# Performance work log

Measured on AMD Instinct MI355X. Metric: run time of the kernel, lower is better.

The kernel has to match this reference:

```python
import jax, jax.numpy as jnp
import numpy as np

MIN_BW = 0.1
MAX_BW = 10.0
BW_FACTOR = 1.0
SAMPLE = 512  # min(512, B) with B >= 512


def _pairwise_dist_sq(a, b):
    # ||a_i - b_j||^2 via GEMM: [N, M], avoids [N, M, D] intermediate
    a2 = jnp.sum(a * a, axis=-1)[:, None]
    b2 = jnp.sum(b * b, axis=-1)[None, :]
    d = a2 + b2 - 2.0 * (a @ b.T)
    return jnp.maximum(d, 0.0)


def _bandwidth(x, y):
    # torch: median heuristic on first SAMPLE rows, under no_grad
    xs = jax.lax.stop_gradient(x[:SAMPLE])
    ys = jax.lax.stop_gradient(y[:SAMPLE])
    dist_sq = _pairwise_dist_sq(xs, ys)
    bw_sq = jnp.median(dist_sq.reshape(-1))
    bw = jnp.sqrt(bw_sq / 2.0) * BW_FACTOR
    return jnp.clip(bw, MIN_BW, MAX_BW)


def setup_inputs() -> dict:
    key = jax.random.key(0)
    kx, ksx, ky, ksy = jax.random.split(key, 4)
    B, D = 4096, 512
    return {
        "x": jax.random.normal(kx, (B, D), dtype=jnp.float32),
        "score_x": jax.random.normal(ksx, (B, D), dtype=jnp.float32),
        "y": jax.random.normal(ky, (B, D), dtype=jnp.float32),
        "score_y": jax.random.normal(ksy, (B, D), dtype=jnp.float32),
    }


def reference(x, score_x, y, score_y):
    D = x.shape[-1]
    h = _bandwidth(x, y)
    h2 = h * h

    dist_sq = _pairwise_dist_sq(x, y)                      # [B, B]
    k = jnp.exp(-dist_sq / (2.0 * h2))                     # [B, B]

    # term1[i,j] = k[i,j] * <score_x_i, score_y_j>
    term1 = k * (score_x @ score_y.T)

    # term2[i,j] = <x_i - y_j, score_y_j> * k[i,j] / h^2
    term2 = ((x @ score_y.T) - jnp.sum(y * score_y, axis=-1)[None, :]) * k / h2

    # term3[i,j] = ||x_i - y_j||^2 * k / h^4 - k * D / h^2
    term3 = dist_sq * k / (h2 * h2) - k * (D / h2)

    return term1 + term2 + term3
```

## Files before the change

### kernel.cpp

```cpp
#include <hip/hip_runtime.h>
#include <hip/hip_bf16.h>

typedef __attribute__((ext_vector_type(8))) short bf16x8;
typedef __attribute__((ext_vector_type(4))) float f32x4;

#define B_N 4096
#define DIM 512
#define HBINS 8192

#define OFF_PARAMS 0
#define OFF_X2     256
#define OFF_Y2     16640
#define OFF_YSY    33024
#define OFF_HIST   49408
#define OFF_TILES  98304
#define MAT_ELEMS  2097152
#define WS_NEED    (OFF_TILES + (size_t)4 * MAT_ELEMS * 2)

static __device__ __forceinline__ unsigned short f2bf_rne(float f) {
    unsigned int u = __float_as_uint(f);
    u += 0x7FFFu + ((u >> 16) & 1u);
    return (unsigned short)(u >> 16);
}
static __device__ __forceinline__ float bf2f(unsigned short h) {
    return __uint_as_float(((unsigned int)h) << 16);
}

static __device__ __forceinline__ int swz(int r, int k) {
    return r * 32 + ((((k >> 3) ^ ((r >> 1) & 3))) << 3) + (k & 7);
}

__global__ __launch_bounds__(256) void k_hist2(
    const float* __restrict__ X, const float* __restrict__ Y,
    unsigned int* __restrict__ hist) {
    __shared__ __align__(16) unsigned short sA[2048];
    __shared__ __align__(16) unsigned short sB[2048];
    __shared__ unsigned int hloc[HBINS];
    __shared__ float x2s[64], y2s[64];

    int t = threadIdx.x;
    int bi = blockIdx.y, bj = blockIdx.x;
    for (int i = t; i < HBINS; i += 256) hloc[i] = 0;

    int lane = t & 63, w = t >> 6;
    int wm = w >> 1, wn = w & 1;
    int fr = lane & 15, fko = (lane >> 4) * 8;

    f32x4 axy[2][2];
#pragma unroll
    for (int i = 0; i < 2; ++i)
#pragma unroll
        for (int j = 0; j < 2; ++j) axy[i][j] = (f32x4)0.f;

    int r = t >> 2, k0 = (t & 3) * 8;
    const float* gx = X + (size_t)(bi * 64 + r) * DIM + k0;
    const float* gy = Y + (size_t)(bj * 64 + r) * DIM + k0;

    int ixA[2], ixB[2];
#pragma unroll
    for (int fm = 0; fm < 2; ++fm) ixA[fm] = swz(wm * 32 + fm * 16 + fr, fko);
#pragma unroll
    for (int fn = 0; fn < 2; ++fn) ixB[fn] = swz(wn * 32 + fn * 16 + fr, fko);

    float na = 0.f, nb = 0.f;
    float4 A0, A1, B0, B1;
#define LDK(kt_) do {                                                       \
        A0 = *(const float4*)(gx + (kt_) * 32);                             \
        A1 = *(const float4*)(gx + (kt_) * 32 + 4);                         \
        B0 = *(const float4*)(gy + (kt_) * 32);                             \
        B1 = *(const float4*)(gy + (kt_) * 32 + 4);                         \
    } while (0)

    LDK(0);
    for (int kt = 0; kt < 16; ++kt) {
        float av[8] = {A0.x, A0.y, A0.z, A0.w, A1.x, A1.y, A1.z, A1.w};
        float bv[8] = {B0.x, B0.y, B0.z, B0.w, B1.x, B1.y, B1.z, B1.w};
        bf16x8 ha, hb;
#pragma unroll
        for (int j = 0; j < 8; ++j) {
            na += av[j] * av[j];
            nb += bv[j] * bv[j];
            ha[j] = (short)f2bf_rne(av[j]);
            hb[j] = (short)f2bf_rne(bv[j]);
        }
        __syncthreads();
        *(bf16x8*)&sA[swz(r, k0)] = ha;
        *(bf16x8*)&sB[swz(r, k0)] = hb;
        if (kt < 15) LDK(kt + 1);
        __syncthreads();

        bf16x8 aX[2];
#pragma unroll
        for (int fm = 0; fm < 2; ++fm) aX[fm] = *(const bf16x8*)&sA[ixA[fm]];
#pragma unroll
        for (int fn = 0; fn < 2; ++fn) {
            bf16x8 bY = *(const bf16x8*)&sB[ixB[fn]];
#pragma unroll
            for (int fm = 0; fm < 2; ++fm)
                axy[fm][fn] = __builtin_amdgcn_mfma_f32_16x16x32_bf16(aX[fm], bY, axy[fm][fn], 0, 0, 0);
        }
    }
#undef LDK

    na += __shfl_xor(na, 1); na += __shfl_xor(na, 2);
    nb += __shfl_xor(nb, 1); nb += __shfl_xor(nb, 2);
    if ((t & 3) == 0) { x2s[r] = na; y2s[r] = nb; }
    __syncthreads();

    int fq = lane >> 4;
#pragma unroll
    for (int fm = 0; fm < 2; ++fm)
#pragma unroll
        for (int fn = 0; fn < 2; ++fn)
#pragma unroll
            for (int rr = 0; rr < 4; ++rr) {
                int rl = wm * 32 + fm * 16 + fq * 4 + rr;
                int cl = wn * 32 + fn * 16 + fr;
                float d = fmaxf(x2s[rl] + y2s[cl] - 2.0f * axy[fm][fn][rr], 0.0f);
                int bin = (int)(d * 4.0f);
                if (bin > HBINS - 1) bin = HBINS - 1;
                atomicAdd(&hloc[bin], 1u);
            }
    __syncthreads();
    for (int i = t; i < HBINS; i += 256) {
        unsigned int v = hloc[i];
        if (v) atomicAdd(&hist[i], v);
    }
}

__global__ __launch_bounds__(256, 1) void k_median(
    const unsigned int* __restrict__ hist, float* __restrict__ params) {
    __shared__ unsigned int hsum[HBINS];
    __shared__ unsigned int part[256];
    __shared__ float vv[2];
    int t = threadIdx.x;
    for (int i = t; i < HBINS / 4; i += 256)
        ((uint4*)hsum)[i] = ((const uint4*)hist)[i];
    __syncthreads();
    unsigned int s = 0;
#pragma unroll 8
    for (int b = t * 32; b < t * 32 + 32; ++b) s += hsum[b];
    part[t] = s;
    __syncthreads();
    unsigned int pre = 0;
    for (int i = 0; i < 256; ++i) {
        unsigned int v = part[i];
        if (i < t) pre += v;
    }
    const unsigned int kk1 = 131072u, kk2 = 131073u;
    unsigned int hi = pre + s;
#pragma unroll
    for (int sel = 0; sel < 2; ++sel) {
        unsigned int kk = sel ? kk2 : kk1;
        if (kk > pre && kk <= hi) {
            unsigned int cc = pre;
            for (int b = 0; b < 32; ++b) {
                cc += hsum[t * 32 + b];
                if (cc >= kk) { vv[sel] = ((float)(t * 32 + b) + 0.5f) * 0.25f; break; }
            }
        }
    }
    __syncthreads();
    if (t == 0) {
        float med = 0.5f * (vv[0] + vv[1]);
        float bw = sqrtf(med * 0.5f);
        bw = fminf(fmaxf(bw, 0.1f), 10.0f);
        float h2 = bw * bw;
        params[0] = 1.0f / (2.0f * h2);
        params[1] = 1.0f / h2;
        params[2] = 1.0f / (h2 * h2);
        params[3] = (float)DIM / h2;
    }
}

__global__ void k_prestats(const float* __restrict__ X, const float* __restrict__ SX,
                           const float* __restrict__ Y, const float* __restrict__ SY,
                           const float* __restrict__ params, unsigned short* __restrict__ tiles,
                           float* __restrict__ x2, float* __restrict__ y2,
                           float* __restrict__ ysy) {
    int side = blockIdx.z;
    const float* P = side ? Y : X;
    const float* Q = side ? SY : SX;
    float c1 = side ? 0.0f : params[1];
    int tile = blockIdx.x, t = threadIdx.x;
    int r = t >> 1;
    int kt = blockIdx.y * 2 + (t & 1);
    const float* gp = P + (size_t)(tile * 128 + r) * DIM + kt * 32;
    const float* gq = Q + (size_t)(tile * 128 + r) * DIM + kt * 32;
    unsigned short* d0 = tiles + (size_t)side * 2 * MAT_ELEMS + (size_t)(tile * 16 + kt) * 4096;
    unsigned short* d1 = d0 + MAT_ELEMS;
    int rt = r >> 4, frl = r & 15;
    float s1 = 0.f, s2 = 0.f;
#pragma unroll
    for (int g = 0; g < 4; ++g) {
        float4 p0 = *(const float4*)(gp + g * 8);
        float4 p1 = *(const float4*)(gp + g * 8 + 4);
        float4 q0 = *(const float4*)(gq + g * 8);
        float4 q1 = *(const float4*)(gq + g * 8 + 4);
        float pv[8] = {p0.x, p0.y, p0.z, p0.w, p1.x, p1.y, p1.z, p1.w};
        float qv[8] = {q0.x, q0.y, q0.z, q0.w, q1.x, q1.y, q1.z, q1.w};
        bf16x8 h0, h1;
#pragma unroll
        for (int j = 0; j < 8; ++j) {
            s1 += pv[j] * pv[j];
            s2 += pv[j] * qv[j];
            h0[j] = (short)f2bf_rne(pv[j]);
            h1[j] = (short)f2bf_rne(qv[j] + c1 * pv[j]);
        }
        *(bf16x8*)&d0[swz(r, g * 8)] = h0;
        *(bf16x8*)&d1[rt * 512 + (g * 16 + frl) * 8] = h1;
    }
    s1 += __shfl_xor(s1, 1);
    s2 += __shfl_xor(s2, 1);
    if ((t & 1) == 0) {
        if (side == 0) {
            atomicAdd(&x2[tile * 128 + r], s1);
        } else {
            atomicAdd(&y2[tile * 128 + r], s1);
            atomicAdd(&ysy[tile * 128 + r], s2);
        }
    }
}

#define GLD(g, l) __builtin_amdgcn_global_load_lds(                                   \
    (const __attribute__((address_space(1))) void*)(g),                               \
    (__attribute__((address_space(3))) void*)(l), 16, 0, 0)

__global__ __launch_bounds__(256, 2) void k_main(
    const unsigned short* __restrict__ tiles,
    const float* __restrict__ x2g, const float* __restrict__ y2g,
    const float* __restrict__ ysyg, const float* __restrict__ params,
    float* __restrict__ out) {
    __shared__ __align__(16) unsigned short sA[2][4096];
    __shared__ __align__(16) unsigned short sB[2][4096];
    __shared__ float x2s[128], y2s[128], ysys[128];

    int t = threadIdx.x;
    int bm = blockIdx.y, bn = blockIdx.x;
    if (t < 128) x2s[t] = x2g[bm * 128 + t];
    else { y2s[t - 128] = y2g[bn * 128 + (t - 128)]; ysys[t - 128] = ysyg[bn * 128 + (t - 128)]; }
    __syncthreads();

    int lane = t & 63, w = t >> 6;
    int wm = w >> 1, wn = w & 1;
    int fr = lane & 15, fko = (lane >> 4) * 8;

    f32x4 axy[4][4], acb[4][4];
#pragma unroll
    for (int i = 0; i < 4; ++i)
#pragma unroll
        for (int j = 0; j < 4; ++j) { axy[i][j] = (f32x4)0.f; acb[i][j] = (f32x4)0.f; }

    const unsigned short* gaX = tiles + (size_t)(bm * 16) * 4096 + t * 8;
    const unsigned short* gbY = tiles + (size_t)2 * MAT_ELEMS + (size_t)(bn * 16) * 4096 + t * 8;
    const unsigned short* gaC = tiles + (size_t)MAT_ELEMS + (size_t)(bm * 16) * 4096
                              + (wm * 4) * 512 + lane * 8;
    const unsigned short* gbS = tiles + (size_t)3 * MAT_ELEMS + (size_t)(bn * 16) * 4096
                              + (wn * 4) * 512 + lane * 8;

#define STAGE(buf, kt_) do {                                                     \
        const unsigned short* pa_ = gaX + (size_t)(kt_) * 4096;                  \
        const unsigned short* pb_ = gbY + (size_t)(kt_) * 4096;                  \
        GLD(pa_,        &sA[buf][t * 8]);                                        \
        GLD(pa_ + 2048, &sA[buf][2048 + t * 8]);                                 \
        GLD(pb_,        &sB[buf][t * 8]);                                        \
        GLD(pb_ + 2048, &sB[buf][2048 + t * 8]);                                 \
    } while (0)

#define FRAGLD(dC, dS, kt_) do {                                                 \
        const unsigned short* pc_ = gaC + (size_t)(kt_) * 4096;                  \
        const unsigned short* ps_ = gbS + (size_t)(kt_) * 4096;                  \
        dC[0] = *(const bf16x8*)(pc_);        dS[0] = *(const bf16x8*)(ps_);     \
        dC[1] = *(const bf16x8*)(pc_ + 512);  dS[1] = *(const bf16x8*)(ps_ + 512);\
        dC[2] = *(const bf16x8*)(pc_ + 1024); dS[2] = *(const bf16x8*)(ps_ + 1024);\
        dC[3] = *(const bf16x8*)(pc_ + 1536); dS[3] = *(const bf16x8*)(ps_ + 1536);\
    } while (0)

    int ixA[4], ixB[4];
#pragma unroll
    for (int fm = 0; fm < 4; ++fm) ixA[fm] = swz(wm * 64 + fm * 16 + fr, fko);
#pragma unroll
    for (int fn = 0; fn < 4; ++fn) ixB[fn] = swz(wn * 64 + fn * 16 + fr, fko);

    bf16x8 fC0[4], fS0[4], fC1[4], fS1[4];

#define KSTEP(CB, CURC, CURS, NXTC, NXTS, NKT, DOPF) do {                        \
        asm volatile("s_waitcnt vmcnt(8)" ::: "memory");   \
        __builtin_amdgcn_sched_barrier(0);                                       \
        __builtin_amdgcn_s_barrier();                                            \
        bf16x8 dX[4], dY[4];                                                     \
        dX[0] = *(const bf16x8*)&sA[CB][ixA[0]];                                 \
        dX[1] = *(const bf16x8*)&sA[CB][ixA[1]];                                 \
        dX[2] = *(const bf16x8*)&sA[CB][ixA[2]];                                 \
        dX[3] = *(const bf16x8*)&sA[CB][ixA[3]];                                 \
        dY[0] = *(const bf16x8*)&sB[CB][ixB[0]];                                 \
        dY[1] = *(const bf16x8*)&sB[CB][ixB[1]];                                 \
        dY[2] = *(const bf16x8*)&sB[CB][ixB[2]];                                 \
        dY[3] = *(const bf16x8*)&sB[CB][ixB[3]];                                 \
        asm volatile("s_waitcnt lgkmcnt(0)" ::: "memory");                       \
        __builtin_amdgcn_sched_barrier(0);                                       \
        __builtin_amdgcn_s_barrier();         \
        if (DOPF) {                                                              \
            STAGE(CB ^ 1, NKT);                                                  \
            FRAGLD(NXTC, NXTS, NKT);                                             \
            asm volatile("s_waitcnt vmcnt(12)" ::: "memory"); \
        } else {                                                                 \
            asm volatile("s_waitcnt vmcnt(0)" ::: "memory");                     \
        }                                                                        \
        __builtin_amdgcn_sched_barrier(0);                                       \
        _Pragma("unroll")                                                        \
        for (int fn_ = 0; fn_ < 4; ++fn_) {                                      \
            _Pragma("unroll")                                                    \
            for (int fm_ = 0; fm_ < 4; ++fm_) {                                  \
                axy[fm_][fn_] = __builtin_amdgcn_mfma_f32_16x16x32_bf16(         \
                    dX[fm_], dY[fn_], axy[fm_][fn_], 0, 0, 0);                   \
                acb[fm_][fn_] = __builtin_amdgcn_mfma_f32_16x16x32_bf16(         \
                    CURC[fm_], CURS[fn_], acb[fm_][fn_], 0, 0, 0);               \
            }                                                                    \
        }                                                                        \
    } while (0)

    STAGE(0, 0);
    FRAGLD(fC0, fS0, 0);

    for (int k2 = 0; k2 < 7; ++k2) {
        KSTEP(0, fC0, fS0, fC1, fS1, 2 * k2 + 1, 1);
        KSTEP(1, fC1, fS1, fC0, fS0, 2 * k2 + 2, 1);
    }
    KSTEP(0, fC0, fS0, fC1, fS1, 15, 1);
    KSTEP(1, fC1, fS1, fC0, fS0, 0, 0);
#undef KSTEP
#undef STAGE
#undef FRAGLD

    float c0 = params[0], c1 = params[1], c2 = params[2], c3 = params[3];
    int fq = lane >> 4;
#pragma unroll
    for (int fm = 0; fm < 4; ++fm) {
#pragma unroll
        for (int fn = 0; fn < 4; ++fn) {
#pragma unroll
            for (int r = 0; r < 4; ++r) {
                int rl = wm * 64 + fm * 16 + fq * 4 + r;
                int cl = wn * 64 + fn * 16 + fr;
                float d = fmaxf(x2s[rl] + y2s[cl] - 2.0f * axy[fm][fn][r], 0.0f);
                float kv = __expf(-d * c0);
                out[(size_t)(bm * 128 + rl) * B_N + (bn * 128 + cl)] =
                    kv * (acb[fm][fn][r] - c1 * ysys[cl] + d * c2 - c3);
            }
        }
    }
}

__global__ void k_rowstats(const float* __restrict__ X, const float* __restrict__ Y,
                           const float* __restrict__ SY,
                           float* __restrict__ x2, float* __restrict__ y2,
                           float* __restrict__ ysy) {
    int t = threadIdx.x;
    int r = blockIdx.x * 4 + (t >> 6);
    int lane = t & 63;
    const float4* px = (const float4*)(X + (size_t)r * DIM) + lane * 2;
    const float4* py = (const float4*)(Y + (size_t)r * DIM) + lane * 2;
    const float4* ps = (const float4*)(SY + (size_t)r * DIM) + lane * 2;
    float4 a0 = px[0], a1 = px[1];
    float4 b0 = py[0], b1 = py[1];
    float4 c0 = ps[0], c1 = ps[1];
    float s1 = a0.x*a0.x + a0.y*a0.y + a0.z*a0.z + a0.w*a0.w
             + a1.x*a1.x + a1.y*a1.y + a1.z*a1.z + a1.w*a1.w;
    float s2 = b0.x*b0.x + b0.y*b0.y + b0.z*b0.z + b0.w*b0.w
             + b1.x*b1.x + b1.y*b1.y + b1.z*b1.z + b1.w*b1.w;
    float s3 = b0.x*c0.x + b0.y*c0.y + b0.z*c0.z + b0.w*c0.w
             + b1.x*c1.x + b1.y*c1.y + b1.z*c1.z + b1.w*c1.w;
#pragma unroll
    for (int o = 32; o > 0; o >>= 1) {
        s1 += __shfl_down(s1, o);
        s2 += __shfl_down(s2, o);
        s3 += __shfl_down(s3, o);
    }
    if (lane == 0) { x2[r] = s1; y2[r] = s2; ysy[r] = s3; }
}

__global__ void k_hist_fp32(const float* __restrict__ X, const float* __restrict__ Y,
                            const float* __restrict__ x2, const float* __restrict__ y2,
                            unsigned int* __restrict__ hist) {
    __shared__ float xs[32][68];
    __shared__ float ys[32][68];
    __shared__ unsigned int hloc[HBINS];
    int t = threadIdx.x;
    for (int i = t; i < HBINS; i += 256) hloc[i] = 0;
    int i0 = blockIdx.y * 32, j0 = blockIdx.x * 32;
    float a00 = 0.f, a01 = 0.f, a10 = 0.f, a11 = 0.f;
    int ti = (t >> 4) * 2, tj = (t & 15) * 2;
    for (int c = 0; c < 8; ++c) {
        __syncthreads();
        int rr = t >> 3, cc = (t & 7) * 8;
        const float* gx = X + (size_t)(i0 + rr) * DIM + c * 64 + cc;
        *(float4*)&xs[rr][cc] = *(const float4*)gx;
        *(float4*)&xs[rr][cc + 4] = *(const float4*)(gx + 4);
        const float* gy = Y + (size_t)(j0 + rr) * DIM + c * 64 + cc;
        *(float4*)&ys[rr][cc] = *(const float4*)gy;
        *(float4*)&ys[rr][cc + 4] = *(const float4*)(gy + 4);
        __syncthreads();
        for (int kk = 0; kk < 64; ++kk) {
            float a0 = xs[ti][kk], a1 = xs[ti + 1][kk];
            float b0 = ys[tj][kk], b1 = ys[tj + 1][kk];
            a00 += a0 * b0; a01 += a0 * b1; a10 += a1 * b0; a11 += a1 * b1;
        }
    }
    float s[2][2] = {{a00, a01}, {a10, a11}};
#pragma unroll
    for (int ii = 0; ii < 2; ++ii)
#pragma unroll
        for (int jj = 0; jj < 2; ++jj) {
            float d = fmaxf(x2[i0 + ti + ii] + y2[j0 + tj + jj] - 2.f * s[ii][jj], 0.f);
            int bin = (int)(d * 4.0f);
            if (bin > HBINS - 1) bin = HBINS - 1;
            atomicAdd(&hloc[bin], 1u);
        }
    __syncthreads();
    for (int i = t; i < HBINS; i += 256) {
        unsigned int v = hloc[i];
        if (v) atomicAdd(&hist[i], v);
    }
}

static __device__ __forceinline__ void store_hi(unsigned short* tile, int r, int k0,
                                                float4 v0, float4 v1) {
    bf16x8 h;
    h[0] = (short)f2bf_rne(v0.x); h[1] = (short)f2bf_rne(v0.y);
    h[2] = (short)f2bf_rne(v0.z); h[3] = (short)f2bf_rne(v0.w);
    h[4] = (short)f2bf_rne(v1.x); h[5] = (short)f2bf_rne(v1.y);
    h[6] = (short)f2bf_rne(v1.z); h[7] = (short)f2bf_rne(v1.w);
    *(bf16x8*)&tile[swz(r, k0)] = h;
}
static __device__ __forceinline__ void store_hilo(unsigned short* th, unsigned short* tl,
                                                  int r, int k0, float4 v0, float4 v1) {
    float f[8] = {v0.x, v0.y, v0.z, v0.w, v1.x, v1.y, v1.z, v1.w};
    bf16x8 h, l;
#pragma unroll
    for (int j = 0; j < 8; ++j) {
        unsigned short hh = f2bf_rne(f[j]);
        h[j] = (short)hh;
        l[j] = (short)f2bf_rne(f[j] - bf2f(hh));
    }
    *(bf16x8*)&th[swz(r, k0)] = h;
    *(bf16x8*)&tl[swz(r, k0)] = l;
}

__global__ __launch_bounds__(256, 2) void k_main_fb(
    const float* __restrict__ X, const float* __restrict__ SX,
    const float* __restrict__ Y, const float* __restrict__ SY,
    const float* __restrict__ x2g, const float* __restrict__ y2g,
    const float* __restrict__ ysyg, const float* __restrict__ params,
    float* __restrict__ out) {
    __shared__ __align__(16) unsigned short tX[4096];
    __shared__ __align__(16) unsigned short tSXH[4096];
    __shared__ __align__(16) unsigned short tSXL[4096];
    __shared__ __align__(16) unsigned short tY[2048];
    __shared__ __align__(16) unsigned short tSYH[2048];
    __shared__ __align__(16) unsigned short tSYL[2048];
    __shared__ float x2s[128];
    __shared__ float y2s[64];
    __shared__ float ysys[64];

    int t = threadIdx.x;
    int bm = blockIdx.y, bn = blockIdx.x;
    if (t < 128) x2s[t] = x2g[bm * 128 + t];
    else if (t < 192) y2s[t - 128] = y2g[bn * 64 + (t - 128)];
    else ysys[t - 192] = ysyg[bn * 64 + (t - 192)];

    int lane = t & 63, w = t >> 6, wm = w >> 1, wn = w & 1;
    f32x4 axy[4][2], ass[4][2], axsy[4][2];
#pragma unroll
    for (int i = 0; i < 4; ++i)
#pragma unroll
        for (int j = 0; j < 2; ++j) {
            axy[i][j] = (f32x4)0.f; ass[i][j] = (f32x4)0.f; axsy[i][j] = (f32x4)0.f;
        }

    for (int kt = 0; kt < DIM / 32; ++kt) {
        int kb = kt * 32;
#pragma unroll
        for (int h = 0; h < 2; ++h) {
            int s = t + h * 256;
            int r = s >> 2, k0 = (s & 3) * 8;
            const float* gx = X + (size_t)(bm * 128 + r) * DIM + kb + k0;
            store_hi(tX, r, k0, *(const float4*)gx, *(const float4*)(gx + 4));
            const float* gs = SX + (size_t)(bm * 128 + r) * DIM + kb + k0;
            store_hilo(tSXH, tSXL, r, k0, *(const float4*)gs, *(const float4*)(gs + 4));
        }
        {
            int r = t >> 2, k0 = (t & 3) * 8;
            const float* gy = Y + (size_t)(bn * 64 + r) * DIM + kb + k0;
            store_hi(tY, r, k0, *(const float4*)gy, *(const float4*)(gy + 4));
            const float* gq = SY + (size_t)(bn * 64 + r) * DIM + kb + k0;
            store_hilo(tSYH, tSYL, r, k0, *(const float4*)gq, *(const float4*)(gq + 4));
        }
        __syncthreads();

        int fr = lane & 15, fk = (lane >> 4) * 8;
        bf16x8 aX[4], aSH[4], aSL[4];
#pragma unroll
        for (int fm = 0; fm < 4; ++fm) {
            int ix = swz(wm * 64 + fm * 16 + fr, fk);
            aX[fm] = *(const bf16x8*)&tX[ix];
            aSH[fm] = *(const bf16x8*)&tSXH[ix];
            aSL[fm] = *(const bf16x8*)&tSXL[ix];
        }
#pragma unroll
        for (int fn = 0; fn < 2; ++fn) {
            int iy = swz(wn * 32 + fn * 16 + fr, fk);
            bf16x8 bY = *(const bf16x8*)&tY[iy];
            bf16x8 bH = *(const bf16x8*)&tSYH[iy];
            bf16x8 bL = *(const bf16x8*)&tSYL[iy];
#pragma unroll
            for (int fm = 0; fm < 4; ++fm) {
                axy[fm][fn] = __builtin_amdgcn_mfma_f32_16x16x32_bf16(aX[fm], bY, axy[fm][fn], 0, 0, 0);
                ass[fm][fn] = __builtin_amdgcn_mfma_f32_16x16x32_bf16(aSH[fm], bH, ass[fm][fn], 0, 0, 0);
                ass[fm][fn] = __builtin_amdgcn_mfma_f32_16x16x32_bf16(aSH[fm], bL, ass[fm][fn], 0, 0, 0);
                ass[fm][fn] = __builtin_amdgcn_mfma_f32_16x16x32_bf16(aSL[fm], bH, ass[fm][fn], 0, 0, 0);
                axsy[fm][fn] = __builtin_amdgcn_mfma_f32_16x16x32_bf16(aX[fm], bH, axsy[fm][fn], 0, 0, 0);
            }
        }
        __syncthreads();
    }

    float c0 = params[0], c1 = params[1], c2 = params[2], c3 = params[3];
    int fr = lane & 15, fq = lane >> 4;
#pragma unroll
    for (int fm = 0; fm < 4; ++fm)
#pragma unroll
        for (int fn = 0; fn < 2; ++fn)
#pragma unroll
            for (int r = 0; r < 4; ++r) {
                int rl = wm * 64 + fm * 16 + fq * 4 + r;
                int cl = wn * 32 + fn * 16 + fr;
                float d = fmaxf(x2s[rl] + y2s[cl] - 2.0f * axy[fm][fn][r], 0.0f);
                float kv = __expf(-d * c0);
                out[(size_t)(bm * 128 + rl) * B_N + (bn * 64 + cl)] =
                    kv * ass[fm][fn][r] + (axsy[fm][fn][r] - ysys[cl]) * (kv * c1)
                    + d * kv * c2 - kv * c3;
            }
}

extern "C" void kernel_launch(void* const* d_in, const int* in_sizes, int n_in,
                              void* d_out, int out_size, void* d_ws, size_t ws_size,
                              hipStream_t stream) {
    const float* x  = (const float*)d_in[0];
    const float* sx = (const float*)d_in[1];
    const float* y  = (const float*)d_in[2];
    const float* sy = (const float*)d_in[3];
    float* out = (float*)d_out;
    char* ws = (char*)d_ws;
    float* params = (float*)(ws + OFF_PARAMS);
    float* x2 = (float*)(ws + OFF_X2);
    float* y2 = (float*)(ws + OFF_Y2);
    float* ysy = (float*)(ws + OFF_YSY);
    unsigned int* hist = (unsigned int*)(ws + OFF_HIST);
    unsigned short* tiles = (unsigned short*)(ws + OFF_TILES);

    if (ws_size >= WS_NEED) {
        hipMemsetAsync(ws + OFF_X2, 0, 3 * 16384 + HBINS * 4, stream);
        k_hist2<<<dim3(8, 8), dim3(256), 0, stream>>>(x, y, hist);
        k_median<<<1, 256, 0, stream>>>(hist, params);
        k_prestats<<<dim3(32, 8, 2), dim3(256), 0, stream>>>(x, sx, y, sy, params, tiles,
                                                             x2, y2, ysy);
        k_main<<<dim3(32, 32), dim3(256), 0, stream>>>(tiles, x2, y2, ysy, params, out);
    } else {
        hipMemsetAsync(hist, 0, HBINS * 4, stream);
        k_rowstats<<<B_N / 4, 256, 0, stream>>>(x, y, sy, x2, y2, ysy);
        k_hist_fp32<<<dim3(16, 16), dim3(256), 0, stream>>>(x, y, x2, y2, hist);
        k_median<<<1, 256, 0, stream>>>(hist, params);
        k_main_fb<<<dim3(64, 32), dim3(256), 0, stream>>>(x, sx, y, sy, x2, y2, ysy, params, out);
    }
}
```

Measured before the change: 93.54 us.

## Coalesce prestats tile writes and issue next-stage prefetch before LDS reads

The prestats kernel is restructured so each thread writes contiguous 16-byte chunks of the destination tiles, with the source index permuted to match the swizzle. Loads of the score operand are skipped where they are not needed, and row sums are reduced across four lanes. In the main GEMM loop, the next stage's global-to-LDS copy and fragment loads are issued right after the first barrier, before the current LDS reads, removing the second barrier. The MFMA block is wrapped in raised wave priority. The early prefetch relies on the double buffer staying race-free with only one barrier per step.

```diff
diff --git a/kernel.cpp b/kernel.cpp
--- a/kernel.cpp
+++ b/kernel.cpp
@@ -183,41 +183,80 @@
     const float* Q = side ? SY : SX;
     float c1 = side ? 0.0f : params[1];
     int tile = blockIdx.x, t = threadIdx.x;
-    int r = t >> 1;
-    int kt = blockIdx.y * 2 + (t & 1);
-    const float* gp = P + (size_t)(tile * 128 + r) * DIM + kt * 32;
-    const float* gq = Q + (size_t)(tile * 128 + r) * DIM + kt * 32;
-    unsigned short* d0 = tiles + (size_t)side * 2 * MAT_ELEMS + (size_t)(tile * 16 + kt) * 4096;
-    unsigned short* d1 = d0 + MAT_ELEMS;
-    int rt = r >> 4, frl = r & 15;
-    float s1 = 0.f, s2 = 0.f;
-#pragma unroll
-    for (int g = 0; g < 4; ++g) {
-        float4 p0 = *(const float4*)(gp + g * 8);
-        float4 p1 = *(const float4*)(gp + g * 8 + 4);
-        float4 q0 = *(const float4*)(gq + g * 8);
-        float4 q1 = *(const float4*)(gq + g * 8 + 4);
-        float pv[8] = {p0.x, p0.y, p0.z, p0.w, p1.x, p1.y, p1.z, p1.w};
-        float qv[8] = {q0.x, q0.y, q0.z, q0.w, q1.x, q1.y, q1.z, q1.w};
-        bf16x8 h0, h1;
-#pragma unroll
-        for (int j = 0; j < 8; ++j) {
-            s1 += pv[j] * pv[j];
-            s2 += pv[j] * qv[j];
-            h0[j] = (short)f2bf_rne(pv[j]);
-            h1[j] = (short)f2bf_rne(qv[j] + c1 * pv[j]);
-        }
-        *(bf16x8*)&d0[swz(r, g * 8)] = h0;
-        *(bf16x8*)&d1[rt * 512 + (g * 16 + frl) * 8] = h1;
-    }
-    s1 += __shfl_xor(s1, 1);
-    s2 += __shfl_xor(s2, 1);
-    if ((t & 1) == 0) {
-        if (side == 0) {
-            atomicAdd(&x2[tile * 128 + r], s1);
-        } else {
-            atomicAdd(&y2[tile * 128 + r], s1);
-            atomicAdd(&ysy[tile * 128 + r], s2);
+    unsigned short* base0 = tiles + (size_t)side * 2 * MAT_ELEMS;
+    unsigned short* base1 = base0 + MAT_ELEMS;
+
+#pragma unroll
+    for (int kt2 = 0; kt2 < 2; ++kt2) {
+        int kt = blockIdx.y * 2 + kt2;
+        unsigned short* d0 = base0 + (size_t)(tile * 16 + kt) * 4096;
+        unsigned short* d1 = base1 + (size_t)(tile * 16 + kt) * 4096;
+
+#pragma unroll
+        for (int c = 0; c < 2; ++c) {
+            int u = c * 256 + t;
+            int r = u >> 2;
+            int k = (((u & 3) ^ ((u >> 3) & 3))) << 3;
+            const float* gp = P + (size_t)(tile * 128 + r) * DIM + kt * 32 + k;
+            float4 p0 = *(const float4*)gp;
+            float4 p1 = *(const float4*)(gp + 4);
+            float pv[8] = {p0.x, p0.y, p0.z, p0.w, p1.x, p1.y, p1.z, p1.w};
+            float s1 = 0.f, s2 = 0.f;
+            bf16x8 h0;
+            if (side) {
+                const float* gq = Q + (size_t)(tile * 128 + r) * DIM + kt * 32 + k;
+                float4 q0 = *(const float4*)gq;
+                float4 q1 = *(const float4*)(gq + 4);
+                float qv[8] = {q0.x, q0.y, q0.z, q0.w, q1.x, q1.y, q1.z, q1.w};
+#pragma unroll
+                for (int j = 0; j < 8; ++j) {
+                    s1 += pv[j] * pv[j];
+                    s2 += pv[j] * qv[j];
+                    h0[j] = (short)f2bf_rne(pv[j]);
+                }
+            } else {
+#pragma unroll
+                for (int j = 0; j < 8; ++j) {
+                    s1 += pv[j] * pv[j];
+                    h0[j] = (short)f2bf_rne(pv[j]);
+                }
+            }
+            *(bf16x8*)&d0[u * 8] = h0;
+            s1 += __shfl_xor(s1, 1); s1 += __shfl_xor(s1, 2);
+            if (side) { s2 += __shfl_xor(s2, 1); s2 += __shfl_xor(s2, 2); }
+            if ((t & 3) == 0) {
+                int row = tile * 128 + r;
+                if (side == 0) {
+                    atomicAdd(&x2[row], s1);
+                } else {
+                    atomicAdd(&y2[row], s1);
+                    atomicAdd(&ysy[row], s2);
+                }
+            }
+        }
+
+#pragma unroll
+        for (int c = 0; c < 2; ++c) {
+            int v = c * 256 + t;
+            int r = (v >> 6) * 16 + (v & 15);
+            int k = ((v >> 4) & 3) << 3;
+            const float* gq = Q + (size_t)(tile * 128 + r) * DIM + kt * 32 + k;
+            float4 q0 = *(const float4*)gq;
+            float4 q1 = *(const float4*)(gq + 4);
+            float qv[8] = {q0.x, q0.y, q0.z, q0.w, q1.x, q1.y, q1.z, q1.w};
+            bf16x8 h1;
+            if (side == 0) {
+                const float* gp = P + (size_t)(tile * 128 + r) * DIM + kt * 32 + k;
+                float4 p0 = *(const float4*)gp;
+                float4 p1 = *(const float4*)(gp + 4);
+                float pv[8] = {p0.x, p0.y, p0.z, p0.w, p1.x, p1.y, p1.z, p1.w};
+#pragma unroll
+                for (int j = 0; j < 8; ++j) h1[j] = (short)f2bf_rne(qv[j] + c1 * pv[j]);
+            } else {
+#pragma unroll
+                for (int j = 0; j < 8; ++j) h1[j] = (short)f2bf_rne(qv[j]);
+            }
+            *(bf16x8*)&d1[v * 8] = h1;
         }
     }
 }
@@ -288,6 +327,10 @@
         asm volatile("s_waitcnt vmcnt(8)" ::: "memory");   \
         __builtin_amdgcn_sched_barrier(0);                                       \
         __builtin_amdgcn_s_barrier();                                            \
+        if (DOPF) {                                                              \
+            STAGE(CB ^ 1, NKT);                                                  \
+            FRAGLD(NXTC, NXTS, NKT);                                             \
+        }                                                                        \
         bf16x8 dX[4], dY[4];                                                     \
         dX[0] = *(const bf16x8*)&sA[CB][ixA[0]];                                 \
         dX[1] = *(const bf16x8*)&sA[CB][ixA[1]];                                 \
@@ -299,15 +342,10 @@
         dY[3] = *(const bf16x8*)&sB[CB][ixB[3]];                                 \
         asm volatile("s_waitcnt lgkmcnt(0)" ::: "memory");                       \
         __builtin_amdgcn_sched_barrier(0);                                       \
-        __builtin_amdgcn_s_barrier();         \
-        if (DOPF) {                                                              \
-            STAGE(CB ^ 1, NKT);                                                  \
-            FRAGLD(NXTC, NXTS, NKT);                                             \
-            asm volatile("s_waitcnt vmcnt(12)" ::: "memory"); \
-        } else {                                                                 \
-            asm volatile("s_waitcnt vmcnt(0)" ::: "memory");                     \
-        }                                                                        \
+        if (DOPF) { asm volatile("s_waitcnt vmcnt(16)" ::: "memory"); }          \
+        else      { asm volatile("s_waitcnt vmcnt(0)" ::: "memory"); }           \
         __builtin_amdgcn_sched_barrier(0);                                       \
+        __builtin_amdgcn_s_setprio(1);                                           \
         _Pragma("unroll")                                                        \
         for (int fn_ = 0; fn_ < 4; ++fn_) {                                      \
             _Pragma("unroll")                                                    \
@@ -318,6 +356,7 @@
                     CURC[fm_], CURS[fn_], acb[fm_][fn_], 0, 0, 0);               \
             }                                                                    \
         }                                                                        \
+        __builtin_amdgcn_s_setprio(0);                                           \
     } while (0)
 
     STAGE(0, 0);
```

Result: faster. 85.50 us (-8.6%).
